# Kernel optimization log

Measured on AMD Instinct MI355X. Metric: run time of the kernel, lower is better.

Reference implementation:

```python
import jax, jax.numpy as jnp
import numpy as np

NEG = -1000000000.0

def setup_inputs() -> dict:
    key = jax.random.key(0)
    k1, k2, k3, k4 = jax.random.split(key, 4)
    B, S, D = 8, 4096, 256
    query = jax.random.normal(k1, (B, S, D), dtype=jnp.float32)
    k_ = jax.random.normal(k2, (B, S, D), dtype=jnp.float32)
    value = jax.random.normal(k3, (B, S, D), dtype=jnp.float32)
    mask = jax.random.bernoulli(k4, 0.1, (B, S, 1))  # True = masked
    return {"query": query, "key": k_, "value": value, "mask": mask}

def reference(query, key, value, mask):
    # a: [B,S,1] sum of squares of query; b: [B,S,1] for key
    a = jnp.sum(query * query, axis=-1, keepdims=True)
    b = jnp.sum(key * key, axis=-1, keepdims=True)
    # s1 = (K^T / b) @ V  -> [B, D, D]; divide each key row s by b_s
    s1 = jnp.einsum('bsd,bse->bde', key / b, value)
    # score = Q / a, masked rows set to -1e9
    score = query / a
    score = jnp.where(mask, NEG, score)
    s2 = jnp.einsum('bsd,bde->bse', score, s1)
    return s2 / query.shape[-1]
```

## Files before the change

kernel.cpp:

```cpp
#include <hip/hip_runtime.h>

#define BB 8
#define SS 4096
#define DD 256
#define NEGV -1000000000.0f
#define NCH (SS / 32)
#define SPLIT 16

typedef float f32x4 __attribute__((ext_vector_type(4)));
typedef short s16x8 __attribute__((ext_vector_type(8)));

static __device__ __forceinline__ unsigned short f2bf(float x) {
  unsigned int u = __builtin_bit_cast(unsigned int, x);
  u += 0x7fffu + ((u >> 16) & 1u);
  return (unsigned short)(u >> 16);
}
static __device__ __forceinline__ float bf2f(unsigned short h) {
  return __builtin_bit_cast(float, (unsigned int)h << 16);
}

static __device__ __forceinline__ void gload_lds16(
    const unsigned short* __restrict__ g, unsigned short* l) {
  __builtin_amdgcn_global_load_lds(
      (const __attribute__((address_space(1))) void*)g,
      (__attribute__((address_space(3))) void*)l, 16, 0, 0);
}

__global__ __launch_bounds__(256, 4) void prep_kernel(
    const float* __restrict__ K, const float* __restrict__ V,
    unsigned short* __restrict__ KT, unsigned short* __restrict__ VT) {
  __shared__ unsigned short tile[32 * 260];
  const int b = blockIdx.y;
  const int sc = blockIdx.x;
  const int s0 = sc * 32;
  const int tid = threadIdx.x;
  const int w = tid >> 6, l = tid & 63;
  const int isK = (blockIdx.z == 0);
  const float* __restrict__ src = isK ? K : V;
  unsigned short* __restrict__ dst = isK ? KT : VT;

  float4 reg[8];
  float ps[8];
#pragma unroll
  for (int it = 0; it < 8; ++it) {
    const int row = it * 4 + w;
    reg[it] = *(const float4*)(src + ((size_t)b * SS + s0 + row) * DD + l * 4);
  }
#pragma unroll
  for (int it = 0; it < 8; ++it)
    ps[it] = reg[it].x * reg[it].x + reg[it].y * reg[it].y +
             reg[it].z * reg[it].z + reg[it].w * reg[it].w;
  float scl[8];
  if (isK) {
#pragma unroll
    for (int off = 32; off; off >>= 1)
#pragma unroll
      for (int it = 0; it < 8; ++it) ps[it] += __shfl_xor(ps[it], off);
#pragma unroll
    for (int it = 0; it < 8; ++it) scl[it] = 1.0f / ps[it];
  } else {
#pragma unroll
    for (int it = 0; it < 8; ++it) scl[it] = 1.0f;
  }
#pragma unroll
  for (int it = 0; it < 8; ++it) {
    const int row = it * 4 + w;
    ushort4 o;
    o.x = f2bf(reg[it].x * scl[it]);
    o.y = f2bf(reg[it].y * scl[it]);
    o.z = f2bf(reg[it].z * scl[it]);
    o.w = f2bf(reg[it].w * scl[it]);
    *(ushort4*)(tile + row * 260 + l * 4) = o;
  }
  __syncthreads();
  const size_t gbase = ((size_t)(b * NCH + sc) * DD + tid) * 32;
#pragma unroll
  for (int c = 0; c < 4; ++c) {
    union { unsigned short h[8]; uint4 v; } u;
#pragma unroll
    for (int j = 0; j < 8; ++j) u.h[j] = tile[(c * 8 + j) * 260 + tid];
    *(uint4*)(dst + gbase + c * 8) = u.v;
  }
}

__global__ __launch_bounds__(256) void p2_kernel(
    const unsigned short* __restrict__ KT, const unsigned short* __restrict__ VT,
    unsigned short* __restrict__ part, int iters) {
  __shared__ unsigned short vt_l[2][128 * 32];
  __shared__ unsigned short kt_l[2][128 * 32];
  const int b = blockIdx.z;
  const int d0 = (blockIdx.x & 1) * 128;
  const int e0 = (blockIdx.x >> 1) * 128;
  const int tid = threadIdx.x;
  const int w = tid >> 6, l = tid & 63;
  const int wr = w & 1, wc = w >> 1;
  const int quad = l >> 4, mr = l & 15;

  f32x4 acc[4][4];
#pragma unroll
  for (int i = 0; i < 4; ++i)
#pragma unroll
    for (int j = 0; j < 4; ++j) acc[i][j] = (f32x4){0.f, 0.f, 0.f, 0.f};

  for (int ks = 0; ks < iters; ++ks) {
    const int c0 = (blockIdx.y * iters + ks) * 2;
#pragma unroll
    for (int h = 0; h < 2; ++h) {
      const size_t vch = ((size_t)(b * NCH + c0 + h) * DD + e0) * 32 + l * 8;
      const size_t kch = ((size_t)(b * NCH + c0 + h) * DD + d0) * 32 + l * 8;
#pragma unroll
      for (int g = 0; g < 2; ++g) {
        const int r0 = w * 32 + g * 16;
        gload_lds16(VT + vch + (size_t)r0 * 32, &vt_l[h][r0 * 32]);
        gload_lds16(KT + kch + (size_t)r0 * 32, &kt_l[h][r0 * 32]);
      }
    }
    __syncthreads();
#pragma unroll
    for (int kh = 0; kh < 2; ++kh) {
      s16x8 af[4], bfr[4];
#pragma unroll
      for (int i = 0; i < 4; ++i)
        af[i] = *(const s16x8*)(&vt_l[kh][(wr * 64 + i * 16 + mr) * 32 + quad * 8]);
#pragma unroll
      for (int j = 0; j < 4; ++j)
        bfr[j] = *(const s16x8*)(&kt_l[kh][(wc * 64 + j * 16 + mr) * 32 + quad * 8]);
#pragma unroll
      for (int i = 0; i < 4; ++i)
#pragma unroll
        for (int j = 0; j < 4; ++j)
          acc[i][j] = __builtin_amdgcn_mfma_f32_16x16x32_bf16(af[i], bfr[j],
                                                              acc[i][j], 0, 0, 0);
    }
    __syncthreads();
  }

  unsigned short* pb = part + ((size_t)blockIdx.y * BB + b) * DD * DD;
#pragma unroll
  for (int i = 0; i < 4; ++i) {
    const int e = e0 + wr * 64 + i * 16 + quad * 4;
#pragma unroll
    for (int j = 0; j < 4; ++j) {
      const int d = d0 + wc * 64 + j * 16 + mr;
      unsigned short* p = pb + (size_t)e * DD + d;
#pragma unroll
      for (int r = 0; r < 4; ++r) p[(size_t)r * DD] = f2bf(acc[i][j][r]);
    }
  }
}

__global__ __launch_bounds__(256) void reduce_kernel(
    const unsigned short* __restrict__ part, unsigned short* __restrict__ s1b,
    float* __restrict__ colsum) {
  const int tid = threadIdx.x;
  const size_t i8 = ((size_t)blockIdx.x * 256 + tid) * 8;
  float a[8];
#pragma unroll
  for (int j = 0; j < 8; ++j) a[j] = 0.f;
  for (int p = 0; p < SPLIT; ++p) {
    union { uint4 v; unsigned short h[8]; } u;
    u.v = *(const uint4*)(part + (size_t)p * (BB * DD * DD) + i8);
#pragma unroll
    for (int j = 0; j < 8; ++j) a[j] += bf2f(u.h[j]);
  }
  union { uint4 v; unsigned short h[8]; } o;
#pragma unroll
  for (int j = 0; j < 8; ++j) o.h[j] = f2bf(a[j]);
  *(uint4*)(s1b + i8) = o.v;
  float rp = (a[0] + a[1]) + (a[2] + a[3]) + ((a[4] + a[5]) + (a[6] + a[7]));
  rp += __shfl_xor(rp, 1);
  rp += __shfl_xor(rp, 2);
  rp += __shfl_xor(rp, 4);
  rp += __shfl_xor(rp, 8);
  rp += __shfl_xor(rp, 16);
  if ((tid & 31) == 0) {
    const int e = (int)((i8 >> 8) & 255);
    const int bb = (int)(i8 >> 16);
    colsum[bb * DD + e] = rp;
  }
}

__global__ __launch_bounds__(256) void p3_kernel(
    const float* __restrict__ Q, const int* __restrict__ mask,
    const unsigned short* __restrict__ s1b, const float* __restrict__ colsum,
    float* __restrict__ out) {
  __shared__ unsigned short qs_l[2][128 * 32 + 16];
  __shared__ unsigned short s1_l[2][128 * 32];
  __shared__ float ps_l[128];
  __shared__ float ca_l[128];
  __shared__ float cs_l[128];
  const int b = blockIdx.z;
  const int e0 = blockIdx.x * 128;
  const int s0 = blockIdx.y * 128;
  const int tid = threadIdx.x;
  const int w = tid >> 6, l = tid & 63;
  const int wr = w & 1, wc = w >> 1;
  const int quad = l >> 4, mr = l & 15;
  const int lr = l >> 2;
  const int lc = (l & 3) * 8;
  const int rg = tid >> 4;
  const int c4 = tid & 15;

  if (tid < 128) cs_l[tid] = colsum[b * DD + e0 + tid];

  f32x4 acc[4][4];
#pragma unroll
  for (int i = 0; i < 4; ++i)
#pragma unroll
    for (int j = 0; j < 4; ++j) acc[i][j] = (f32x4){0.f, 0.f, 0.f, 0.f};
  float np[8];
#pragma unroll
  for (int u = 0; u < 8; ++u) np[u] = 0.f;

  for (int ks = 0; ks < 4; ++ks) {
    const int dc = ks * 64;
#pragma unroll
    for (int h = 0; h < 2; ++h)
#pragma unroll
      for (int g = 0; g < 2; ++g) {
        const int r0 = w * 32 + g * 16;
        gload_lds16(s1b + ((size_t)b * DD + e0 + r0 + lr) * DD + dc + h * 32 + lc,
                    &s1_l[h][r0 * 32]);
      }
    float4 qv[8];
#pragma unroll
    for (int u = 0; u < 8; ++u) {
      const int row = rg + u * 16;
      qv[u] = *(const float4*)(Q + ((size_t)b * SS + s0 + row) * DD + dc + c4 * 4);
    }
#pragma unroll
    for (int u = 0; u < 8; ++u) {
      np[u] += qv[u].x * qv[u].x + qv[u].y * qv[u].y + qv[u].z * qv[u].z +
               qv[u].w * qv[u].w;
      ushort4 o;
      o.x = f2bf(qv[u].x); o.y = f2bf(qv[u].y);
      o.z = f2bf(qv[u].z); o.w = f2bf(qv[u].w);
      *(ushort4*)&qs_l[c4 >> 3][(rg + u * 16) * 32 + (c4 & 7) * 4] = o;
    }
    __syncthreads();
#pragma unroll
    for (int kh = 0; kh < 2; ++kh) {
      s16x8 af[4], bfr[4];
#pragma unroll
      for (int i = 0; i < 4; ++i)
        af[i] = *(const s16x8*)(&qs_l[kh][(wr * 64 + i * 16 + mr) * 32 + quad * 8]);
#pragma unroll
      for (int j = 0; j < 4; ++j)
        bfr[j] = *(const s16x8*)(&s1_l[kh][(wc * 64 + j * 16 + mr) * 32 + quad * 8]);
#pragma unroll
      for (int i = 0; i < 4; ++i)
#pragma unroll
        for (int j = 0; j < 4; ++j)
          acc[i][j] = __builtin_amdgcn_mfma_f32_16x16x32_bf16(af[i], bfr[j],
                                                              acc[i][j], 0, 0, 0);
    }
    __syncthreads();
  }

#pragma unroll
  for (int u = 0; u < 8; ++u) {
    np[u] += __shfl_xor(np[u], 1);
    np[u] += __shfl_xor(np[u], 2);
    np[u] += __shfl_xor(np[u], 4);
    np[u] += __shfl_xor(np[u], 8);
  }
  if (c4 == 0) {
#pragma unroll
    for (int u = 0; u < 8; ++u) ps_l[rg + u * 16] = np[u];
  }
  __syncthreads();
  if (tid < 128) {
    const int mk = mask[b * SS + s0 + tid];
    ca_l[tid] = mk ? 0.0f : (1.0f / ps_l[tid]);
  }
  __syncthreads();

#pragma unroll
  for (int i = 0; i < 4; ++i) {
#pragma unroll
    for (int j = 0; j < 4; ++j) {
      const int el = wc * 64 + j * 16 + mr;
      const float csum = cs_l[el];
      float* p = out + ((size_t)b * SS + s0 + wr * 64 + i * 16 + quad * 4) * DD +
                 e0 + el;
#pragma unroll
      for (int r = 0; r < 4; ++r) {
        const float ca = ca_l[wr * 64 + i * 16 + quad * 4 + r];
        const float val = (ca != 0.0f) ? acc[i][j][r] * ca : NEGV * csum;
        p[(size_t)r * DD] = val * (1.0f / DD);
      }
    }
  }
}

extern "C" void kernel_launch(void* const* d_in, const int* in_sizes, int n_in,
                              void* d_out, int out_size, void* d_ws,
                              size_t ws_size, hipStream_t stream) {
  const float* Q = (const float*)d_in[0];
  const float* K = (const float*)d_in[1];
  const float* V = (const float*)d_in[2];
  const int* mask = (const int*)d_in[3];
  float* out = (float*)d_out;

  char* ws = (char*)d_ws;
  const size_t MB = (size_t)1024 * 1024;
  unsigned short* KT = (unsigned short*)(ws);
  unsigned short* VT = (unsigned short*)(ws + 16 * MB);
  unsigned short* part = (unsigned short*)(ws + 32 * MB);
  unsigned short* s1b = (unsigned short*)(ws + 48 * MB);
  float* colsum = (float*)(ws + 49 * MB);

  const int iters = SS / (64 * SPLIT);

  prep_kernel<<<dim3(SS / 32, BB, 2), 256, 0, stream>>>(K, V, KT, VT);
  p2_kernel<<<dim3(4, SPLIT, BB), 256, 0, stream>>>(KT, VT, part, iters);
  reduce_kernel<<<dim3(BB * DD * DD / (8 * 256)), 256, 0, stream>>>(part, s1b,
                                                                    colsum);
  p3_kernel<<<dim3(2, SS / 128, BB), 256, 0, stream>>>(Q, mask, s1b, colsum,
                                                       out);
}
```

Measured before the change: 170.0 us.

## Double-buffer Q and S1 LDS tiles in p3 kernel to overlap loads with MFMA

```diff
diff --git a/kernel.cpp b/kernel.cpp
--- a/kernel.cpp
+++ b/kernel.cpp
@@ -184,8 +184,8 @@
     const float* __restrict__ Q, const int* __restrict__ mask,
     const unsigned short* __restrict__ s1b, const float* __restrict__ colsum,
     float* __restrict__ out) {
-  __shared__ unsigned short qs_l[2][128 * 32 + 16];
-  __shared__ unsigned short s1_l[2][128 * 32];
+  __shared__ unsigned short qs_l[2][2][128 * 32 + 16];
+  __shared__ unsigned short s1_l[2][2][128 * 32];
   __shared__ float ps_l[128];
   __shared__ float ca_l[128];
   __shared__ float cs_l[128];
@@ -212,7 +212,7 @@
 #pragma unroll
   for (int u = 0; u < 8; ++u) np[u] = 0.f;
 
-  for (int ks = 0; ks < 4; ++ks) {
+  auto stageS1 = [&](int buf, int ks) {
     const int dc = ks * 64;
 #pragma unroll
     for (int h = 0; h < 2; ++h)
@@ -220,14 +220,18 @@
       for (int g = 0; g < 2; ++g) {
         const int r0 = w * 32 + g * 16;
         gload_lds16(s1b + ((size_t)b * DD + e0 + r0 + lr) * DD + dc + h * 32 + lc,
-                    &s1_l[h][r0 * 32]);
+                    &s1_l[buf][h][r0 * 32]);
       }
-    float4 qv[8];
+  };
+  auto loadQ = [&](int ks, float4* qv) {
+    const int dc = ks * 64;
 #pragma unroll
     for (int u = 0; u < 8; ++u) {
       const int row = rg + u * 16;
       qv[u] = *(const float4*)(Q + ((size_t)b * SS + s0 + row) * DD + dc + c4 * 4);
     }
+  };
+  auto writeQ = [&](int buf, const float4* qv) {
 #pragma unroll
     for (int u = 0; u < 8; ++u) {
       np[u] += qv[u].x * qv[u].x + qv[u].y * qv[u].y + qv[u].z * qv[u].z +
@@ -235,18 +239,31 @@
       ushort4 o;
       o.x = f2bf(qv[u].x); o.y = f2bf(qv[u].y);
       o.z = f2bf(qv[u].z); o.w = f2bf(qv[u].w);
-      *(ushort4*)&qs_l[c4 >> 3][(rg + u * 16) * 32 + (c4 & 7) * 4] = o;
-    }
-    __syncthreads();
+      *(ushort4*)&qs_l[buf][c4 >> 3][(rg + u * 16) * 32 + (c4 & 7) * 4] = o;
+    }
+  };
+
+  float4 qvA[8], qvB[8];
+  stageS1(0, 0);
+  loadQ(0, qvA);
+  writeQ(0, qvA);
+  __syncthreads();
+
+  for (int ks = 0; ks < 4; ++ks) {
+    const int cur = ks & 1;
+    if (ks < 3) {
+      stageS1(cur ^ 1, ks + 1);
+      loadQ(ks + 1, qvB);
+    }
 #pragma unroll
     for (int kh = 0; kh < 2; ++kh) {
       s16x8 af[4], bfr[4];
 #pragma unroll
       for (int i = 0; i < 4; ++i)
-        af[i] = *(const s16x8*)(&qs_l[kh][(wr * 64 + i * 16 + mr) * 32 + quad * 8]);
+        af[i] = *(const s16x8*)(&qs_l[cur][kh][(wr * 64 + i * 16 + mr) * 32 + quad * 8]);
 #pragma unroll
       for (int j = 0; j < 4; ++j)
-        bfr[j] = *(const s16x8*)(&s1_l[kh][(wc * 64 + j * 16 + mr) * 32 + quad * 8]);
+        bfr[j] = *(const s16x8*)(&s1_l[cur][kh][(wc * 64 + j * 16 + mr) * 32 + quad * 8]);
 #pragma unroll
       for (int i = 0; i < 4; ++i)
 #pragma unroll
@@ -254,6 +271,7 @@
           acc[i][j] = __builtin_amdgcn_mfma_f32_16x16x32_bf16(af[i], bfr[j],
                                                               acc[i][j], 0, 0, 0);
     }
+    if (ks < 3) writeQ(cur ^ 1, qvB);
     __syncthreads();
   }
 
```

Measured after the change: 170.6 us. No clear change (+0.4%).

## Halve p2/p3 tile sizes and remap 1D grids with XCD-aware block swizzle

Applied to the files above, without the earlier changes.

```diff
diff --git a/kernel.cpp b/kernel.cpp
--- a/kernel.cpp
+++ b/kernel.cpp
@@ -87,23 +87,28 @@
     const unsigned short* __restrict__ KT, const unsigned short* __restrict__ VT,
     unsigned short* __restrict__ part, int iters) {
   __shared__ unsigned short vt_l[2][128 * 32];
-  __shared__ unsigned short kt_l[2][128 * 32];
-  const int b = blockIdx.z;
-  const int d0 = (blockIdx.x & 1) * 128;
-  const int e0 = (blockIdx.x >> 1) * 128;
+  __shared__ unsigned short kt_l[2][64 * 32];
+  const int id = blockIdx.x;
+  const int xcd = id & 7, slot = id >> 3;
+  const int xx = slot & 7;
+  const int G = xcd * 16 + (slot >> 3);
+  const int yy = G & 15;
+  const int b = G >> 4;
+  const int e0 = (xx & 1) * 128;
+  const int d0 = (xx >> 1) * 64;
   const int tid = threadIdx.x;
   const int w = tid >> 6, l = tid & 63;
   const int wr = w & 1, wc = w >> 1;
   const int quad = l >> 4, mr = l & 15;
 
-  f32x4 acc[4][4];
+  f32x4 acc[4][2];
 #pragma unroll
   for (int i = 0; i < 4; ++i)
 #pragma unroll
-    for (int j = 0; j < 4; ++j) acc[i][j] = (f32x4){0.f, 0.f, 0.f, 0.f};
+    for (int j = 0; j < 2; ++j) acc[i][j] = (f32x4){0.f, 0.f, 0.f, 0.f};
 
   for (int ks = 0; ks < iters; ++ks) {
-    const int c0 = (blockIdx.y * iters + ks) * 2;
+    const int c0 = (yy * iters + ks) * 2;
 #pragma unroll
     for (int h = 0; h < 2; ++h) {
       const size_t vch = ((size_t)(b * NCH + c0 + h) * DD + e0) * 32 + l * 8;
@@ -112,36 +117,37 @@
       for (int g = 0; g < 2; ++g) {
         const int r0 = w * 32 + g * 16;
         gload_lds16(VT + vch + (size_t)r0 * 32, &vt_l[h][r0 * 32]);
-        gload_lds16(KT + kch + (size_t)r0 * 32, &kt_l[h][r0 * 32]);
       }
+      const int rk = w * 16;
+      gload_lds16(KT + kch + (size_t)rk * 32, &kt_l[h][rk * 32]);
     }
     __syncthreads();
 #pragma unroll
     for (int kh = 0; kh < 2; ++kh) {
-      s16x8 af[4], bfr[4];
+      s16x8 af[4], bfr[2];
 #pragma unroll
       for (int i = 0; i < 4; ++i)
         af[i] = *(const s16x8*)(&vt_l[kh][(wr * 64 + i * 16 + mr) * 32 + quad * 8]);
 #pragma unroll
-      for (int j = 0; j < 4; ++j)
-        bfr[j] = *(const s16x8*)(&kt_l[kh][(wc * 64 + j * 16 + mr) * 32 + quad * 8]);
+      for (int j = 0; j < 2; ++j)
+        bfr[j] = *(const s16x8*)(&kt_l[kh][(wc * 32 + j * 16 + mr) * 32 + quad * 8]);
 #pragma unroll
       for (int i = 0; i < 4; ++i)
 #pragma unroll
-        for (int j = 0; j < 4; ++j)
+        for (int j = 0; j < 2; ++j)
           acc[i][j] = __builtin_amdgcn_mfma_f32_16x16x32_bf16(af[i], bfr[j],
                                                               acc[i][j], 0, 0, 0);
     }
     __syncthreads();
   }
 
-  unsigned short* pb = part + ((size_t)blockIdx.y * BB + b) * DD * DD;
+  unsigned short* pb = part + ((size_t)yy * BB + b) * DD * DD;
 #pragma unroll
   for (int i = 0; i < 4; ++i) {
     const int e = e0 + wr * 64 + i * 16 + quad * 4;
 #pragma unroll
-    for (int j = 0; j < 4; ++j) {
-      const int d = d0 + wc * 64 + j * 16 + mr;
+    for (int j = 0; j < 2; ++j) {
+      const int d = d0 + wc * 32 + j * 16 + mr;
       unsigned short* p = pb + (size_t)e * DD + d;
 #pragma unroll
       for (int r = 0; r < 4; ++r) p[(size_t)r * DD] = f2bf(acc[i][j][r]);
@@ -184,14 +190,17 @@
     const float* __restrict__ Q, const int* __restrict__ mask,
     const unsigned short* __restrict__ s1b, const float* __restrict__ colsum,
     float* __restrict__ out) {
-  __shared__ unsigned short qs_l[2][128 * 32 + 16];
+  __shared__ unsigned short qs_l[2][64 * 32 + 16];
   __shared__ unsigned short s1_l[2][128 * 32];
-  __shared__ float ps_l[128];
-  __shared__ float ca_l[128];
+  __shared__ float ps_l[64];
+  __shared__ float ca_l[64];
   __shared__ float cs_l[128];
-  const int b = blockIdx.z;
-  const int e0 = blockIdx.x * 128;
-  const int s0 = blockIdx.y * 128;
+  const int id = blockIdx.x;
+  const int xcd = id & 7, slot = id >> 3;
+  const int e0 = (slot & 1) * 128;
+  const int G = xcd * 64 + (slot >> 1);
+  const int s0 = (G & 63) * 64;
+  const int b = G >> 6;
   const int tid = threadIdx.x;
   const int w = tid >> 6, l = tid & 63;
   const int wr = w & 1, wc = w >> 1;
@@ -203,14 +212,14 @@
 
   if (tid < 128) cs_l[tid] = colsum[b * DD + e0 + tid];
 
-  f32x4 acc[4][4];
-#pragma unroll
-  for (int i = 0; i < 4; ++i)
+  f32x4 acc[2][4];
+#pragma unroll
+  for (int i = 0; i < 2; ++i)
 #pragma unroll
     for (int j = 0; j < 4; ++j) acc[i][j] = (f32x4){0.f, 0.f, 0.f, 0.f};
-  float np[8];
-#pragma unroll
-  for (int u = 0; u < 8; ++u) np[u] = 0.f;
+  float np[4];
+#pragma unroll
+  for (int u = 0; u < 4; ++u) np[u] = 0.f;
 
   for (int ks = 0; ks < 4; ++ks) {
     const int dc = ks * 64;
@@ -222,14 +231,14 @@
         gload_lds16(s1b + ((size_t)b * DD + e0 + r0 + lr) * DD + dc + h * 32 + lc,
                     &s1_l[h][r0 * 32]);
       }
-    float4 qv[8];
-#pragma unroll
-    for (int u = 0; u < 8; ++u) {
+    float4 qv[4];
+#pragma unroll
+    for (int u = 0; u < 4; ++u) {
       const int row = rg + u * 16;
       qv[u] = *(const float4*)(Q + ((size_t)b * SS + s0 + row) * DD + dc + c4 * 4);
     }
 #pragma unroll
-    for (int u = 0; u < 8; ++u) {
+    for (int u = 0; u < 4; ++u) {
       np[u] += qv[u].x * qv[u].x + qv[u].y * qv[u].y + qv[u].z * qv[u].z +
                qv[u].w * qv[u].w;
       ushort4 o;
@@ -240,15 +249,15 @@
     __syncthreads();
 #pragma unroll
     for (int kh = 0; kh < 2; ++kh) {
-      s16x8 af[4], bfr[4];
-#pragma unroll
-      for (int i = 0; i < 4; ++i)
-        af[i] = *(const s16x8*)(&qs_l[kh][(wr * 64 + i * 16 + mr) * 32 + quad * 8]);
+      s16x8 af[2], bfr[4];
+#pragma unroll
+      for (int i = 0; i < 2; ++i)
+        af[i] = *(const s16x8*)(&qs_l[kh][(wr * 32 + i * 16 + mr) * 32 + quad * 8]);
 #pragma unroll
       for (int j = 0; j < 4; ++j)
         bfr[j] = *(const s16x8*)(&s1_l[kh][(wc * 64 + j * 16 + mr) * 32 + quad * 8]);
 #pragma unroll
-      for (int i = 0; i < 4; ++i)
+      for (int i = 0; i < 2; ++i)
 #pragma unroll
         for (int j = 0; j < 4; ++j)
           acc[i][j] = __builtin_amdgcn_mfma_f32_16x16x32_bf16(af[i], bfr[j],
@@ -258,7 +267,7 @@
   }
 
 #pragma unroll
-  for (int u = 0; u < 8; ++u) {
+  for (int u = 0; u < 4; ++u) {
     np[u] += __shfl_xor(np[u], 1);
     np[u] += __shfl_xor(np[u], 2);
     np[u] += __shfl_xor(np[u], 4);
@@ -266,26 +275,26 @@
   }
   if (c4 == 0) {
 #pragma unroll
-    for (int u = 0; u < 8; ++u) ps_l[rg + u * 16] = np[u];
+    for (int u = 0; u < 4; ++u) ps_l[rg + u * 16] = np[u];
   }
   __syncthreads();
-  if (tid < 128) {
+  if (tid < 64) {
     const int mk = mask[b * SS + s0 + tid];
     ca_l[tid] = mk ? 0.0f : (1.0f / ps_l[tid]);
   }
   __syncthreads();
 
 #pragma unroll
-  for (int i = 0; i < 4; ++i) {
+  for (int i = 0; i < 2; ++i) {
 #pragma unroll
     for (int j = 0; j < 4; ++j) {
       const int el = wc * 64 + j * 16 + mr;
       const float csum = cs_l[el];
-      float* p = out + ((size_t)b * SS + s0 + wr * 64 + i * 16 + quad * 4) * DD +
+      float* p = out + ((size_t)b * SS + s0 + wr * 32 + i * 16 + quad * 4) * DD +
                  e0 + el;
 #pragma unroll
       for (int r = 0; r < 4; ++r) {
-        const float ca = ca_l[wr * 64 + i * 16 + quad * 4 + r];
+        const float ca = ca_l[wr * 32 + i * 16 + quad * 4 + r];
         const float val = (ca != 0.0f) ? acc[i][j][r] * ca : NEGV * csum;
         p[(size_t)r * DD] = val * (1.0f / DD);
       }
@@ -313,9 +322,8 @@
   const int iters = SS / (64 * SPLIT);
 
   prep_kernel<<<dim3(SS / 32, BB, 2), 256, 0, stream>>>(K, V, KT, VT);
-  p2_kernel<<<dim3(4, SPLIT, BB), 256, 0, stream>>>(KT, VT, part, iters);
+  p2_kernel<<<dim3(1024), 256, 0, stream>>>(KT, VT, part, iters);
   reduce_kernel<<<dim3(BB * DD * DD / (8 * 256)), 256, 0, stream>>>(part, s1b,
                                                                     colsum);
-  p3_kernel<<<dim3(2, SS / 128, BB), 256, 0, stream>>>(Q, mask, s1b, colsum,
-                                                       out);
-}
+  p3_kernel<<<dim3(1024), 256, 0, stream>>>(Q, mask, s1b, colsum, out);
+}
```

Result: slower. 174.7 us (+2.7%).
